# Performance work log

Hardware: AMD Instinct MI355X
Metric: run time of the kernel (lower is better)

## Reference

```python
import jax, jax.numpy as jnp
import numpy as np

N_NODES = 8192
N_EDGES = 49152
IN_F, HID, H1, H2, OUT_F = 128, 64, 64, 5, 32
N_BONDS = 64


def setup_inputs() -> dict:
    key = jax.random.key(0)
    ks = jax.random.split(key, 12)
    s = 0.05
    return {
        "x": jax.random.normal(ks[0], (N_NODES, IN_F), jnp.float32),
        "edge_index": jax.random.randint(ks[1], (2, N_EDGES), 0, N_NODES, jnp.int32),
        "lefts": jax.random.randint(ks[2], (N_BONDS,), 0, N_NODES, jnp.int32),
        "rights": jax.random.randint(ks[3], (N_BONDS,), 0, N_NODES, jnp.int32),
        "W1": jax.random.normal(ks[4], (H1 * HID, IN_F), jnp.float32) * s,
        "att_src1": jax.random.normal(ks[5], (H1, HID), jnp.float32) * s,
        "att_dst1": jax.random.normal(ks[6], (H1, HID), jnp.float32) * s,
        "b1": jnp.zeros((H1 * HID,), jnp.float32),
        "W2": jax.random.normal(ks[7], (H2 * OUT_F, H1 * HID), jnp.float32) * s,
        "att_src2": jax.random.normal(ks[8], (H2, OUT_F), jnp.float32) * s,
        "att_dst2": jax.random.normal(ks[9], (H2, OUT_F), jnp.float32) * s,
        "b2": jnp.zeros((OUT_F,), jnp.float32),
    }


def _gat_conv(x, src, dst, W, a_src, a_dst, b, concat):
    # x: [N, F_in]; W: [H*C, F_in]; a_src/a_dst: [H, C]
    N = x.shape[0]
    H, C = a_src.shape
    h = (x @ W.T).reshape(N, H, C)                    # [N, H, C]
    alpha_s = jnp.einsum("nhc,hc->nh", h, a_src)      # [N, H]
    alpha_d = jnp.einsum("nhc,hc->nh", h, a_dst)
    logits = jax.nn.leaky_relu(alpha_s[src] + alpha_d[dst], negative_slope=0.2)  # [E, H]
    # scatter-softmax over incoming edges of each destination node
    m = jax.ops.segment_max(logits, dst, num_segments=N)
    e = jnp.exp(logits - m[dst])
    denom = jax.ops.segment_sum(e, dst, num_segments=N)
    alpha = e / denom[dst]                            # [E, H]
    msg = h[src] * alpha[:, :, None]                  # [E, H, C]
    out = jax.ops.segment_sum(msg, dst, num_segments=N)  # [N, H, C]
    out = out.reshape(N, H * C) if concat else out.mean(axis=1)
    return out + b


def reference(x, edge_index, lefts, rights, W1, att_src1, att_dst1, b1,
              W2, att_src2, att_dst2, b2):
    N = x.shape[0]
    loops = jnp.arange(N, dtype=edge_index.dtype)
    src = jnp.concatenate([edge_index[0], loops])
    dst = jnp.concatenate([edge_index[1], loops])
    x1 = jax.nn.elu(_gat_conv(x, src, dst, W1, att_src1, att_dst1, b1, concat=True))
    x2 = _gat_conv(x1, src, dst, W2, att_src2, att_dst2, b2, concat=False)  # [N, OUT_F]
    score = (x2[lefts] + x2[rights]).sum(axis=-1)     # [N_BONDS]
    return jax.nn.softmax(score, axis=0)
```

## Files before the change

### kernel.cpp

```cpp
#include <hip/hip_runtime.h>
#include <hip/hip_bf16.h>
#include <math.h>

#define N_NODES  8192
#define N_EDGES  49152
#define E_TOT    57344
#define IN_F     128
#define HID      64
#define NH1      64
#define NH2      5
#define OUT_F    32
#define F1       4096
#define F2       160
#define N_BONDS  64
#define ET       16
#define NP       4
#define HG       16

typedef short bf16x8 __attribute__((ext_vector_type(8)));
typedef float f32x4  __attribute__((ext_vector_type(4)));

__device__ __forceinline__ float lrelu(float x){ return x > 0.f ? x : 0.2f*x; }

__device__ __forceinline__ unsigned short bf16_rne(float f){
    unsigned u = __float_as_uint(f);
    unsigned r = u + 0x7FFF + ((u >> 16) & 1);
    return (unsigned short)(r >> 16);
}
__device__ __forceinline__ float bf16f(unsigned short h){
    return __uint_as_float((unsigned)h << 16);
}

__device__ __forceinline__ void block_sync_lds(){
    asm volatile("s_waitcnt lgkmcnt(0)" ::: "memory");
    __builtin_amdgcn_s_barrier();
    asm volatile("" ::: "memory");
}

__device__ __forceinline__ void gload_lds16(const unsigned short* gp, unsigned short* lp_base){
    __builtin_amdgcn_global_load_lds(
        (const __attribute__((address_space(1))) unsigned int*)(const void*)gp,
        (__attribute__((address_space(3))) unsigned int*)(void*)lp_base,
        16, 0, 0);
}

__global__ void k_init_counts(int* counts){
    int i = blockIdx.x*256 + threadIdx.x;
    if (i < N_NODES) counts[i] = 1;
}
__global__ void k_count(const int* __restrict__ ei, int* counts){
    int i = blockIdx.x*256 + threadIdx.x;
    if (i < N_EDGES) atomicAdd(&counts[ei[N_EDGES + i]], 1);
}
__global__ __launch_bounds__(1024) void k_scan(const int* __restrict__ counts,
                                               int* __restrict__ row_start,
                                               int* __restrict__ cursor){
    __shared__ int sd[1024];
    int t = threadIdx.x;
    int v[8]; int sum = 0;
    #pragma unroll
    for (int i=0;i<8;i++){ v[i] = counts[t*8+i]; sum += v[i]; }
    sd[t] = sum; __syncthreads();
    for (int off=1; off<1024; off<<=1){
        int vv = (t >= off) ? sd[t-off] : 0;
        __syncthreads();
        sd[t] += vv;
        __syncthreads();
    }
    int run = sd[t] - sum;
    #pragma unroll
    for (int i=0;i<8;i++){ row_start[t*8+i] = run; cursor[t*8+i] = run; run += v[i]; }
    if (t == 1023) row_start[N_NODES] = run;
}
__global__ void k_fill(const int* __restrict__ ei, int* cursor, int* __restrict__ csr_src){
    int i = blockIdx.x*256 + threadIdx.x;
    if (i >= E_TOT) return;
    int s, d;
    if (i < N_EDGES){ s = ei[i]; d = ei[N_EDGES + i]; }
    else { s = i - N_EDGES; d = s; }
    int pos = atomicAdd(&cursor[d], 1);
    csr_src[pos] = s;
}

__global__ void k_packw1d(const float* __restrict__ W1,
                          unsigned short* __restrict__ fh, unsigned short* __restrict__ fl){
    int g = blockIdx.x*256 + threadIdx.x;
    int lane = g & 63, ct = (g >> 6) & 3, ks = (g >> 8) & 3, hg = g >> 10;
    int col = hg*64 + ct*16 + (lane & 15);
    int k = ks*32 + (lane >> 4)*8;
    const float* src = W1 + (size_t)col*IN_F + k;
    bf16x8 hv, lv;
    #pragma unroll
    for (int j=0;j<8;j++){
        float f = src[j];
        unsigned short hb = bf16_rne(f);
        hv[j] = (short)hb;
        lv[j] = (short)bf16_rne(f - bf16f(hb));
    }
    *(bf16x8*)(fh + (size_t)g*8) = hv;
    *(bf16x8*)(fl + (size_t)g*8) = lv;
}

__global__ void k_packw2d(const float* __restrict__ W2,
                          unsigned short* __restrict__ fh, unsigned short* __restrict__ fl){
    int g = blockIdx.x*256 + threadIdx.x;
    int lane = g & 63, ni = (g >> 6) % 10, kc = g / 640;
    int n = ni*16 + (lane & 15);
    int k = kc*32 + (lane >> 4)*8;
    const float* src = W2 + (size_t)n*F1 + k;
    bf16x8 hv, lv;
    #pragma unroll
    for (int j=0;j<8;j++){
        float f = src[j];
        unsigned short hb = bf16_rne(f);
        hv[j] = (short)hb;
        lv[j] = (short)bf16_rne(f - bf16f(hb));
    }
    *(bf16x8*)(fh + (size_t)g*8) = hv;
    *(bf16x8*)(fl + (size_t)g*8) = lv;
}

__global__ __launch_bounds__(128) void k_attvec(const float* __restrict__ W1,
        const float* __restrict__ a_s, const float* __restrict__ a_d,
        float* __restrict__ vsT, float* __restrict__ vdT){
    int h = blockIdx.x, k = threadIdx.x;
    float s = 0.f, d = 0.f;
    for (int c = 0; c < HID; c++){
        float w = W1[(size_t)(h*HID + c)*IN_F + k];
        s += a_s[h*HID + c] * w;
        d += a_d[h*HID + c] * w;
    }
    vsT[k*NH1 + h] = s;
    vdT[k*NH1 + h] = d;
}

__global__ __launch_bounds__(128) void k_alpha1x(const float* __restrict__ x,
        const float* __restrict__ vsT, const float* __restrict__ vdT,
        float* __restrict__ as1, float* __restrict__ ad1){
    int n = blockIdx.x, t = threadIdx.x;
    __shared__ float xs[IN_F];
    xs[t] = x[(size_t)n*IN_F + t];
    __syncthreads();
    if (t < NH1){
        float s = 0.f, d = 0.f;
        for (int k = 0; k < IN_F; k++){
            float xv = xs[k];
            s += xv * vsT[k*NH1 + t];
            d += xv * vdT[k*NH1 + t];
        }
        as1[n*NH1 + t] = s;
        ad1[n*NH1 + t] = d;
    }
}

__global__ __launch_bounds__(256) void k_aggx64(const float* __restrict__ x,
        const float* __restrict__ as1, const float* __restrict__ ad1,
        const int* __restrict__ row_start, const int* __restrict__ csr_src,
        unsigned short* __restrict__ txhi){
    int n = blockIdx.x, t = threadIdx.x;
    __shared__ float ad_s[NH1];
    __shared__ float wt[ET][NH1];
    __shared__ int   st[ET];
    __shared__ float xs[ET][IN_F];
    int e0 = row_start[n], e1 = row_start[n+1];
    if (t < NH1) ad_s[t] = ad1[n*NH1 + t];
    int hq = t >> 4, f0 = (t & 15)*8;
    float acc[4][8] = {};
    float D[4] = {0.f, 0.f, 0.f, 0.f};
    for (int eb = e0; eb < e1; eb += ET){
        int ne = min(ET, e1 - eb);
        if (t < ne) st[t] = csr_src[eb + t];
        __syncthreads();
        for (int idx = t; idx < ne*32; idx += 256){
            int e = idx >> 5, f4 = idx & 31;
            *(float4*)&xs[e][f4*4] = *(const float4*)(x + (size_t)st[e]*IN_F + f4*4);
        }
        for (int idx = t; idx < ne*NH1; idx += 256){
            int e = idx >> 6, hh = idx & 63;
            wt[e][hh] = __expf(lrelu(as1[st[e]*NH1 + hh] + ad_s[hh]));
        }
        __syncthreads();
        for (int e = 0; e < ne; e++){
            float4 v0 = *(const float4*)&xs[e][f0];
            float4 v1 = *(const float4*)&xs[e][f0+4];
            float xv[8] = {v0.x,v0.y,v0.z,v0.w,v1.x,v1.y,v1.z,v1.w};
            #pragma unroll
            for (int c=0;c<4;c++){
                float w = wt[e][hq*4 + c];
                D[c] += w;
                #pragma unroll
                for (int j=0;j<8;j++) acc[c][j] += w*xv[j];
            }
        }
        __syncthreads();
    }
    #pragma unroll
    for (int c=0;c<4;c++){
        float dinv = 1.f / D[c];
        bf16x8 hv;
        #pragma unroll
        for (int j=0;j<8;j++) hv[j] = (short)bf16_rne(acc[c][j] * dinv);
        size_t o = ((size_t)(hq*4 + c)*N_NODES + n)*IN_F + f0;
        *(bf16x8*)(txhi + o) = hv;
    }
}

__global__ __launch_bounds__(512, 4) void k_gemm12(
        const unsigned short* __restrict__ txhi,
        const unsigned short* __restrict__ w1fh, const unsigned short* __restrict__ w1fl,
        const unsigned short* __restrict__ w2fh, const unsigned short* __restrict__ w2fl,
        const float* __restrict__ b1,
        float* __restrict__ P){
    __shared__ __attribute__((aligned(16))) unsigned short Als[8192];
    __shared__ __attribute__((aligned(16))) unsigned short W1sh[8192];
    __shared__ __attribute__((aligned(16))) unsigned short W2s[20480];
    __shared__ __attribute__((aligned(16))) unsigned short X1s[4096];

    const int tid  = threadIdx.x;
    const int wave = tid >> 6, lane = tid & 63;
    const int wr = wave >> 1, wc = wave & 1;
    const int q = lane >> 4, l16 = lane & 15;
    const int row0 = blockIdx.x * 64;
    const int g = blockIdx.y;
    const int h0 = g * HG;

    {
        const unsigned short* Ab = txhi + ((size_t)h0*N_NODES + row0)*IN_F;
        const unsigned short* W1b = w1fh + (size_t)h0*8192;
        #pragma unroll
        for (int j=0;j<2;j++){
            int idx = j*8 + wave;
            int eo = idx*512 + lane*8;
            int row = eo >> 7;
            int se = (eo & ~127) | ((eo & 127) ^ ((row & 7) << 3));
            gload_lds16(Ab + se, &Als[idx*512]);
        }
        #pragma unroll
        for (int j=0;j<2;j++){
            int idx = j*8 + wave;
            gload_lds16(W1b + idx*512 + lane*8, &W1sh[idx*512]);
        }
    }

    f32x4 acc2[5] = {};
    bf16x8 wlo[8];

    #pragma unroll 1
    for (int hh = 0; hh < HG; hh++){
        const int h = h0 + hh;
        block_sync_lds();
        {
            const unsigned short* W1lb = w1fl + (size_t)h*8192;
            #pragma unroll
            for (int ks=0;ks<4;ks++)
                #pragma unroll
                for (int ni=0;ni<2;ni++)
                    wlo[ks*2+ni] = *(const bf16x8*)(W1lb + (size_t)(ks*4 + 2*wc + ni)*512 + lane*8);
        }
        asm volatile("" ::: "memory");
        {
            const unsigned short* W2bh = w2fh + (size_t)h*10240;
            const unsigned short* W2bl = w2fl + (size_t)h*10240;
            #pragma unroll
            for (int j=0;j<5;j++){
                int idx = j*8 + wave;
                const unsigned short* src = (idx < 20) ? (W2bh + idx*512 + lane*8)
                                                       : (W2bl + (idx-20)*512 + lane*8);
                gload_lds16(src, &W2s[idx*512]);
            }
        }
        asm volatile("s_waitcnt vmcnt(13)" ::: "memory");
        __builtin_amdgcn_s_barrier();
        const int arow = wr*16 + l16;
        f32x4 c1[2] = {};
        __builtin_amdgcn_s_setprio(1);
        #pragma unroll
        for (int ks=0;ks<4;ks++){
            int sidx = (arow*128 + ks*32 + q*8) ^ ((arow & 7) << 3);
            bf16x8 af = *(const bf16x8*)&Als[sidx];
            #pragma unroll
            for (int ni=0;ni<2;ni++){
                bf16x8 bh = *(const bf16x8*)&W1sh[(ks*4 + 2*wc + ni)*512 + lane*8];
                c1[ni] = __builtin_amdgcn_mfma_f32_16x16x32_bf16(af, bh, c1[ni], 0,0,0);
                c1[ni] = __builtin_amdgcn_mfma_f32_16x16x32_bf16(af, wlo[ks*2+ni], c1[ni], 0,0,0);
            }
        }
        __builtin_amdgcn_s_setprio(0);
        #pragma unroll
        for (int ni=0;ni<2;ni++){
            int col = (2*wc+ni)*16 + l16;
            float b = b1[h*64 + col];
            #pragma unroll
            for (int i=0;i<4;i++){
                float v = c1[ni][i] + b;
                float o = v > 0.f ? v : (__expf(v) - 1.f);
                int row = wr*16 + q*4 + i;
                int sidx = (row*64 + col) ^ ((row & 7) << 3);
                X1s[sidx] = bf16_rne(o);
            }
        }
        asm volatile("s_waitcnt vmcnt(0) lgkmcnt(0)" ::: "memory");
        __builtin_amdgcn_s_barrier();
        if (hh + 1 < HG){
            const unsigned short* Ab = txhi + ((size_t)(h+1)*N_NODES + row0)*IN_F;
            const unsigned short* W1b = w1fh + (size_t)(h+1)*8192;
            #pragma unroll
            for (int j=0;j<2;j++){
                int idx = j*8 + wave;
                int eo = idx*512 + lane*8;
                int row = eo >> 7;
                int se = (eo & ~127) | ((eo & 127) ^ ((row & 7) << 3));
                gload_lds16(Ab + se, &Als[idx*512]);
            }
            #pragma unroll
            for (int j=0;j<2;j++){
                int idx = j*8 + wave;
                gload_lds16(W1b + idx*512 + lane*8, &W1sh[idx*512]);
            }
        }
        const int xrow = wr*16 + l16;
        __builtin_amdgcn_s_setprio(1);
        #pragma unroll
        for (int ks=0;ks<2;ks++){
            int sidx = (xrow*64 + ks*32 + q*8) ^ ((xrow & 7) << 3);
            bf16x8 a2 = *(const bf16x8*)&X1s[sidx];
            #pragma unroll
            for (int ni=0;ni<5;ni++){
                int f = (ks*10 + wc*5 + ni)*512 + lane*8;
                bf16x8 bh = *(const bf16x8*)&W2s[f];
                bf16x8 bl = *(const bf16x8*)&W2s[10240 + f];
                acc2[ni] = __builtin_amdgcn_mfma_f32_16x16x32_bf16(a2, bh, acc2[ni], 0,0,0);
                acc2[ni] = __builtin_amdgcn_mfma_f32_16x16x32_bf16(a2, bl, acc2[ni], 0,0,0);
            }
        }
        __builtin_amdgcn_s_setprio(0);
    }

    float* outp = P + ((size_t)g*N_NODES + row0)*F2;
    #pragma unroll
    for (int ni=0;ni<5;ni++)
        #pragma unroll
        for (int i=0;i<4;i++){
            int rr = wr*16 + q*4 + i;
            int cc = wc*80 + ni*16 + l16;
            outp[(size_t)rr*F2 + cc] = acc2[ni][i];
        }
}

__global__ __launch_bounds__(256) void k_redalpha(const float* __restrict__ P,
        const float* __restrict__ att_s, const float* __restrict__ att_d,
        float* __restrict__ h2, float* __restrict__ as2, float* __restrict__ ad2){
    __shared__ float hs[64][164];
    __shared__ float avs[160], avd[160];
    int b = blockIdx.x, t = threadIdx.x;
    int n0 = b*64;
    if (t < 160){ avs[t] = att_s[t]; avd[t] = att_d[t]; }
    const int NV = N_NODES*F2/4;
    int base = b * (64*F2/4);
    #pragma unroll
    for (int v=0; v<10; v++){
        int i = base + v*256 + t;
        float4 a = ((const float4*)P)[i];
        #pragma unroll
        for (int kb=1; kb<NP; kb++){
            float4 bb = ((const float4*)P)[(size_t)kb*NV + i];
            a.x+=bb.x; a.y+=bb.y; a.z+=bb.z; a.w+=bb.w;
        }
        ((float4*)h2)[i] = a;
        int flat = (v*256 + t)*4;
        int n = flat / F2, c = flat % F2;
        *(float4*)&hs[n][c] = a;
    }
    __syncthreads();
    for (int idx = t; idx < 320; idx += 256){
        int n = idx/5, hh = idx%5;
        const float* hp = &hs[n][hh*32];
        const float* ap = &avs[hh*32];
        const float* dp = &avd[hh*32];
        float s=0.f, d=0.f;
        #pragma unroll
        for (int c=0;c<32;c++){ float hv=hp[c]; s += hv*ap[c]; d += hv*dp[c]; }
        as2[(n0+n)*NH2 + hh] = s;
        ad2[(n0+n)*NH2 + hh] = d;
    }
}

__global__ __launch_bounds__(256) void k_agg2(const float* __restrict__ h2,
        const float* __restrict__ as2, const float* __restrict__ ad2,
        const int* __restrict__ row_start, const int* __restrict__ csr_src,
        const float* __restrict__ b2, float* __restrict__ x2){
    int n = blockIdx.x, t = threadIdx.x;
    __shared__ float ad_s[NH2], den_s[NH2], sacc[F2];
    int e0 = row_start[n], e1 = row_start[n+1];
    if (t < NH2) ad_s[t] = ad2[n*NH2 + t];
    __syncthreads();
    if (t < NH2){
        float d = 0.f;
        for (int e=e0;e<e1;e++){
            int s = csr_src[e];
            d += __expf(lrelu(as2[s*NH2 + t] + ad_s[t]));
        }
        den_s[t] = d;
    }
    __syncthreads();
    if (t < F2){
        int h = t >> 5;
        float adh  = ad_s[h];
        float dinv = 1.f/den_s[h];
        float acc = 0.f;
        for (int e=e0;e<e1;e++){
            int s = csr_src[e];
            float w = __expf(lrelu(as2[s*NH2 + h] + adh)) * dinv;
            acc += w * h2[(size_t)s*F2 + t];
        }
        sacc[t] = acc;
    }
    __syncthreads();
    if (t < OUT_F){
        float v = (sacc[t] + sacc[t+32] + sacc[t+64] + sacc[t+96] + sacc[t+128]) * 0.2f + b2[t];
        x2[n*OUT_F + t] = v;
    }
}

__global__ __launch_bounds__(64) void k_bond(const float* __restrict__ x2,
        const int* __restrict__ lefts, const int* __restrict__ rights,
        float* __restrict__ out){
    int b = threadIdx.x;
    int L = lefts[b], R = rights[b];
    float s = 0.f;
    #pragma unroll
    for (int c=0;c<OUT_F;c+=4){
        float4 l4 = *(const float4*)(x2 + (size_t)L*OUT_F + c);
        float4 r4 = *(const float4*)(x2 + (size_t)R*OUT_F + c);
        s += l4.x+l4.y+l4.z+l4.w + r4.x+r4.y+r4.z+r4.w;
    }
    float m = s;
    #pragma unroll
    for (int off=1; off<64; off<<=1) m = fmaxf(m, __shfl_xor(m, off));
    float e = expf(s - m);
    float sum = e;
    #pragma unroll
    for (int off=1; off<64; off<<=1) sum += __shfl_xor(sum, off);
    out[b] = e / sum;
}

extern "C" void kernel_launch(void* const* d_in, const int* in_sizes, int n_in,
                              void* d_out, int out_size, void* d_ws, size_t ws_size,
                              hipStream_t stream){
    const float* x      = (const float*)d_in[0];
    const int*   ei     = (const int*)  d_in[1];
    const int*   lefts  = (const int*)  d_in[2];
    const int*   rights = (const int*)  d_in[3];
    const float* W1     = (const float*)d_in[4];
    const float* att_s1 = (const float*)d_in[5];
    const float* att_d1 = (const float*)d_in[6];
    const float* b1     = (const float*)d_in[7];
    const float* W2     = (const float*)d_in[8];
    const float* att_s2 = (const float*)d_in[9];
    const float* att_d2 = (const float*)d_in[10];
    const float* b2     = (const float*)d_in[11];
    float* out = (float*)d_out;

    char* ws = (char*)d_ws;
    size_t off = 0;
    auto alloc = [&](size_t bytes) -> void* {
        void* p = ws + off;
        off += (bytes + 255) & ~(size_t)255;
        return p;
    };
    unsigned short* txhi = (unsigned short*)alloc((size_t)NH1*N_NODES*IN_F*2);
    float* part   = (float*)alloc((size_t)NP*N_NODES*F2*4);
    float* h2     = (float*)alloc((size_t)N_NODES*F2*4);
    float* as1    = (float*)alloc((size_t)N_NODES*NH1*4);
    float* ad1    = (float*)alloc((size_t)N_NODES*NH1*4);
    float* as2    = (float*)alloc((size_t)N_NODES*NH2*4);
    float* ad2    = (float*)alloc((size_t)N_NODES*NH2*4);
    float* x2     = (float*)alloc((size_t)N_NODES*OUT_F*4);
    float* vsT    = (float*)alloc((size_t)IN_F*NH1*4);
    float* vdT    = (float*)alloc((size_t)IN_F*NH1*4);
    unsigned short* w1fh = (unsigned short*)alloc((size_t)F1*IN_F*2);
    unsigned short* w1fl = (unsigned short*)alloc((size_t)F1*IN_F*2);
    unsigned short* w2fh = (unsigned short*)alloc((size_t)128*10*512*2);
    unsigned short* w2fl = (unsigned short*)alloc((size_t)128*10*512*2);
    int* counts    = (int*)alloc((size_t)N_NODES*4);
    int* row_start = (int*)alloc((size_t)(N_NODES+1)*4);
    int* cursor    = (int*)alloc((size_t)N_NODES*4);
    int* csr_src   = (int*)alloc((size_t)E_TOT*4);

    k_init_counts<<<32, 256, 0, stream>>>(counts);
    k_count<<<192, 256, 0, stream>>>(ei, counts);
    k_scan<<<1, 1024, 0, stream>>>(counts, row_start, cursor);
    k_fill<<<224, 256, 0, stream>>>(ei, cursor, csr_src);

    k_packw1d<<<65536/256, 256, 0, stream>>>(W1, w1fh, w1fl);
    k_packw2d<<<81920/256, 256, 0, stream>>>(W2, w2fh, w2fl);

    k_attvec<<<NH1, 128, 0, stream>>>(W1, att_s1, att_d1, vsT, vdT);
    k_alpha1x<<<N_NODES, 128, 0, stream>>>(x, vsT, vdT, as1, ad1);

    k_aggx64<<<N_NODES, 256, 0, stream>>>(x, as1, ad1, row_start, csr_src, txhi);

    k_gemm12<<<dim3(128, NP), 512, 0, stream>>>(txhi, w1fh, w1fl, w2fh, w2fl, b1, part);
    k_redalpha<<<128, 256, 0, stream>>>(part, att_s2, att_d2, h2, as2, ad2);

    k_agg2<<<N_NODES, 256, 0, stream>>>(h2, as2, ad2, row_start, csr_src, b2, x2);

    k_bond<<<1, 64, 0, stream>>>(x2, lefts, rights, out);
}
```

Before: 241.7 us.

## Retile fused GEMM warps to 2x4 layout and replace count init with memset

The fused two-layer GEMM kernel changes its wave decomposition from a 4x2 grid (16 rows, two column tiles) to a 2x4 grid (32 rows, one column tile). Each wave now reuses one W1 fragment across two A row tiles, which halves the low-part W1 register preload and its global traffic. The W2 output columns are split unevenly across waves (3,3,2,2 tiles), and the vmcnt wait count is adjusted to match the smaller preload. Separately, the count-initialization kernel is replaced by a hipMemsetAsync, with the self-loop +1 folded into the scan. The risks are wave load imbalance in the second GEMM and more LDS reads of A per wave.

```diff
diff --git a/kernel.cpp b/kernel.cpp
--- a/kernel.cpp
+++ b/kernel.cpp
@@ -44,10 +44,6 @@
         16, 0, 0);
 }
 
-__global__ void k_init_counts(int* counts){
-    int i = blockIdx.x*256 + threadIdx.x;
-    if (i < N_NODES) counts[i] = 1;
-}
 __global__ void k_count(const int* __restrict__ ei, int* counts){
     int i = blockIdx.x*256 + threadIdx.x;
     if (i < N_EDGES) atomicAdd(&counts[ei[N_EDGES + i]], 1);
@@ -59,7 +55,7 @@
     int t = threadIdx.x;
     int v[8]; int sum = 0;
     #pragma unroll
-    for (int i=0;i<8;i++){ v[i] = counts[t*8+i]; sum += v[i]; }
+    for (int i=0;i<8;i++){ v[i] = counts[t*8+i] + 1; sum += v[i]; }
     sd[t] = sum; __syncthreads();
     for (int off=1; off<1024; off<<=1){
         int vv = (t >= off) ? sd[t-off] : 0;
@@ -218,11 +214,12 @@
 
     const int tid  = threadIdx.x;
     const int wave = tid >> 6, lane = tid & 63;
-    const int wr = wave >> 1, wc = wave & 1;
+    const int wr = wave & 1, wc = wave >> 1;
     const int q = lane >> 4, l16 = lane & 15;
     const int row0 = blockIdx.x * 64;
     const int g = blockIdx.y;
     const int h0 = g * HG;
+    const int nbase = (wc < 2) ? wc*3 : 6 + (wc-2)*2;
 
     {
         const unsigned short* Ab = txhi + ((size_t)h0*N_NODES + row0)*IN_F;
@@ -242,8 +239,8 @@
         }
     }
 
-    f32x4 acc2[5] = {};
-    bf16x8 wlo[8];
+    f32x4 acc2[2][3] = {};
+    bf16x8 wlo[4];
 
     #pragma unroll 1
     for (int hh = 0; hh < HG; hh++){
@@ -253,9 +250,7 @@
             const unsigned short* W1lb = w1fl + (size_t)h*8192;
             #pragma unroll
             for (int ks=0;ks<4;ks++)
-                #pragma unroll
-                for (int ni=0;ni<2;ni++)
-                    wlo[ks*2+ni] = *(const bf16x8*)(W1lb + (size_t)(ks*4 + 2*wc + ni)*512 + lane*8);
+                wlo[ks] = *(const bf16x8*)(W1lb + (size_t)(ks*4 + wc)*512 + lane*8);
         }
         asm volatile("" ::: "memory");
         {
@@ -269,34 +264,36 @@
                 gload_lds16(src, &W2s[idx*512]);
             }
         }
-        asm volatile("s_waitcnt vmcnt(13)" ::: "memory");
+        asm volatile("s_waitcnt vmcnt(9)" ::: "memory");
         __builtin_amdgcn_s_barrier();
-        const int arow = wr*16 + l16;
         f32x4 c1[2] = {};
         __builtin_amdgcn_s_setprio(1);
         #pragma unroll
         for (int ks=0;ks<4;ks++){
-            int sidx = (arow*128 + ks*32 + q*8) ^ ((arow & 7) << 3);
-            bf16x8 af = *(const bf16x8*)&Als[sidx];
-            #pragma unroll
-            for (int ni=0;ni<2;ni++){
-                bf16x8 bh = *(const bf16x8*)&W1sh[(ks*4 + 2*wc + ni)*512 + lane*8];
-                c1[ni] = __builtin_amdgcn_mfma_f32_16x16x32_bf16(af, bh, c1[ni], 0,0,0);
-                c1[ni] = __builtin_amdgcn_mfma_f32_16x16x32_bf16(af, wlo[ks*2+ni], c1[ni], 0,0,0);
+            bf16x8 bh = *(const bf16x8*)&W1sh[(ks*4 + wc)*512 + lane*8];
+            #pragma unroll
+            for (int mi=0;mi<2;mi++){
+                int arow = wr*32 + mi*16 + l16;
+                int sidx = (arow*128 + ks*32 + q*8) ^ ((arow & 7) << 3);
+                bf16x8 af = *(const bf16x8*)&Als[sidx];
+                c1[mi] = __builtin_amdgcn_mfma_f32_16x16x32_bf16(af, bh, c1[mi], 0,0,0);
+                c1[mi] = __builtin_amdgcn_mfma_f32_16x16x32_bf16(af, wlo[ks], c1[mi], 0,0,0);
             }
         }
         __builtin_amdgcn_s_setprio(0);
-        #pragma unroll
-        for (int ni=0;ni<2;ni++){
-            int col = (2*wc+ni)*16 + l16;
+        {
+            int col = wc*16 + l16;
             float b = b1[h*64 + col];
             #pragma unroll
-            for (int i=0;i<4;i++){
-                float v = c1[ni][i] + b;
-                float o = v > 0.f ? v : (__expf(v) - 1.f);
-                int row = wr*16 + q*4 + i;
-                int sidx = (row*64 + col) ^ ((row & 7) << 3);
-                X1s[sidx] = bf16_rne(o);
+            for (int mi=0;mi<2;mi++){
+                #pragma unroll
+                for (int i=0;i<4;i++){
+                    float v = c1[mi][i] + b;
+                    float o = v > 0.f ? v : (__expf(v) - 1.f);
+                    int row = wr*32 + mi*16 + q*4 + i;
+                    int sidx = (row*64 + col) ^ ((row & 7) << 3);
+                    X1s[sidx] = bf16_rne(o);
+                }
             }
         }
         asm volatile("s_waitcnt vmcnt(0) lgkmcnt(0)" ::: "memory");
@@ -318,19 +315,40 @@
                 gload_lds16(W1b + idx*512 + lane*8, &W1sh[idx*512]);
             }
         }
-        const int xrow = wr*16 + l16;
         __builtin_amdgcn_s_setprio(1);
         #pragma unroll
         for (int ks=0;ks<2;ks++){
-            int sidx = (xrow*64 + ks*32 + q*8) ^ ((xrow & 7) << 3);
-            bf16x8 a2 = *(const bf16x8*)&X1s[sidx];
-            #pragma unroll
-            for (int ni=0;ni<5;ni++){
-                int f = (ks*10 + wc*5 + ni)*512 + lane*8;
-                bf16x8 bh = *(const bf16x8*)&W2s[f];
-                bf16x8 bl = *(const bf16x8*)&W2s[10240 + f];
-                acc2[ni] = __builtin_amdgcn_mfma_f32_16x16x32_bf16(a2, bh, acc2[ni], 0,0,0);
-                acc2[ni] = __builtin_amdgcn_mfma_f32_16x16x32_bf16(a2, bl, acc2[ni], 0,0,0);
+            bf16x8 a2[2];
+            #pragma unroll
+            for (int mi=0;mi<2;mi++){
+                int row = wr*32 + mi*16 + l16;
+                int sidx = (row*64 + ks*32 + q*8) ^ ((row & 7) << 3);
+                a2[mi] = *(const bf16x8*)&X1s[sidx];
+            }
+            if (wc < 2){
+                #pragma unroll
+                for (int ni=0;ni<3;ni++){
+                    int f = (ks*10 + nbase + ni)*512 + lane*8;
+                    bf16x8 bh = *(const bf16x8*)&W2s[f];
+                    bf16x8 bl = *(const bf16x8*)&W2s[10240 + f];
+                    #pragma unroll
+                    for (int mi=0;mi<2;mi++){
+                        acc2[mi][ni] = __builtin_amdgcn_mfma_f32_16x16x32_bf16(a2[mi], bh, acc2[mi][ni], 0,0,0);
+                        acc2[mi][ni] = __builtin_amdgcn_mfma_f32_16x16x32_bf16(a2[mi], bl, acc2[mi][ni], 0,0,0);
+                    }
+                }
+            } else {
+                #pragma unroll
+                for (int ni=0;ni<2;ni++){
+                    int f = (ks*10 + nbase + ni)*512 + lane*8;
+                    bf16x8 bh = *(const bf16x8*)&W2s[f];
+                    bf16x8 bl = *(const bf16x8*)&W2s[10240 + f];
+                    #pragma unroll
+                    for (int mi=0;mi<2;mi++){
+                        acc2[mi][ni] = __builtin_amdgcn_mfma_f32_16x16x32_bf16(a2[mi], bh, acc2[mi][ni], 0,0,0);
+                        acc2[mi][ni] = __builtin_amdgcn_mfma_f32_16x16x32_bf16(a2[mi], bl, acc2[mi][ni], 0,0,0);
+                    }
+                }
             }
         }
         __builtin_amdgcn_s_setprio(0);
@@ -338,12 +356,16 @@
 
     float* outp = P + ((size_t)g*N_NODES + row0)*F2;
     #pragma unroll
-    for (int ni=0;ni<5;ni++)
-        #pragma unroll
-        for (int i=0;i<4;i++){
-            int rr = wr*16 + q*4 + i;
-            int cc = wc*80 + ni*16 + l16;
-            outp[(size_t)rr*F2 + cc] = acc2[ni][i];
+    for (int mi=0;mi<2;mi++)
+        #pragma unroll
+        for (int ni=0;ni<3;ni++){
+            if (wc >= 2 && ni >= 2) continue;
+            #pragma unroll
+            for (int i=0;i<4;i++){
+                int rr = wr*32 + mi*16 + q*4 + i;
+                int cc = (nbase + ni)*16 + l16;
+                outp[(size_t)rr*F2 + cc] = acc2[mi][ni][i];
+            }
         }
 }
 
@@ -487,7 +509,7 @@
     int* cursor    = (int*)alloc((size_t)N_NODES*4);
     int* csr_src   = (int*)alloc((size_t)E_TOT*4);
 
-    k_init_counts<<<32, 256, 0, stream>>>(counts);
+    hipMemsetAsync(counts, 0, (size_t)N_NODES*4, stream);
     k_count<<<192, 256, 0, stream>>>(ei, counts);
     k_scan<<<1, 1024, 0, stream>>>(counts, row_start, cursor);
     k_fill<<<224, 256, 0, stream>>>(ei, cursor, csr_src);
```

After: 241.8 us. No clear change (+0.0%).
